# Kernel optimization log

Hardware: AMD Instinct MI355X
Metric: run time of the kernel (lower is better)

Reference implementation:

```python
import jax, jax.numpy as jnp
import numpy as np

# Involution2D config (matches init_kwargs)
F = 256          # filters
K = 3            # kernel_size
G = 16           # groups
RR = 4           # reduce_ratio
BN_EPS = 1e-3    # keras BatchNormalization default epsilon


def setup_inputs() -> dict:
    key = jax.random.key(0)
    ks = jax.random.split(key, 8)
    C = 256
    Cr = F // RR                    # reduce_mapping channels = 64
    KKG = K * K * G                 # span_mapping channels = 144
    s = lambda k, sh, fan: jax.random.normal(k, sh, jnp.float32) * (1.0 / np.sqrt(fan))
    return {
        "x": jax.random.normal(ks[0], (4, 128, 128, C), jnp.float32),
        # reduce_mapping: 1x1 conv + BN(inference) + relu
        "Wr": s(ks[1], (C, Cr), C),
        "br": jnp.zeros((Cr,), jnp.float32),
        "gamma": jnp.ones((Cr,), jnp.float32),
        "beta": jnp.zeros((Cr,), jnp.float32),
        "mean": jax.random.normal(ks[2], (Cr,), jnp.float32) * 0.1,
        "var": jax.random.uniform(ks[3], (Cr,), jnp.float32, 0.5, 1.5),
        # span_mapping: 1x1 conv -> K*K*G dynamic weights
        "Ws": s(ks[4], (Cr, KKG), Cr),
        "bs": jnp.zeros((KKG,), jnp.float32),
        # initial_mapping: 1x1 conv -> F (applied since F != K*K*G)
        "Wi": s(ks[5], (C, F), C),
        "bi": jnp.zeros((F,), jnp.float32),
    }


def reference(x, Wr, br, gamma, beta, mean, var, Ws, bs, Wi, bi):
    B, H, W, _ = x.shape
    KK = K * K
    # reduce_mapping: 1x1 conv + BN(inference) + relu
    r = jnp.einsum('bhwc,cd->bhwd', x, Wr) + br
    r = jax.nn.relu((r - mean) * jax.lax.rsqrt(var + BN_EPS) * gamma + beta)
    # span_mapping: per-pixel dynamic kernel weights [B,H,W,KK*G] -> [B,H,W,G,1,KK]
    w = jnp.einsum('bhwd,dk->bhwk', r, Ws) + bs
    w = w.reshape(B, H, W, G, KK)[:, :, :, :, None, :]
    # initial_mapping: 1x1 conv -> F channels
    xi = jnp.einsum('bhwc,cf->bhwf', x, Wi) + bi
    # tf.image.extract_patches (SAME, stride=1, rate=1): layout is
    # (kernel_pos major, channel minor), i.e. flat index = kpos*F + c
    pad = (K - 1) // 2
    xp = jnp.pad(xi, ((0, 0), (pad, pad), (pad, pad), (0, 0)))
    patches = jnp.stack(
        [xp[:, i:i + H, j:j + W, :] for i in range(K) for j in range(K)],
        axis=3)                                   # [B,H,W,KK,F]
    # faithful to the original K.reshape of the flat [KK*F] axis
    patches = patches.reshape(B, H, W, G, F // G, KK)
    out = jnp.sum(w * patches, axis=-1)           # [B,H,W,G,F//G]
    return out.reshape(B, H, W, F)
```

## Files before the change

### kernel.cpp

```cpp
#include <hip/hip_runtime.h>

#define BN_EPS 1e-3f

typedef __attribute__((ext_vector_type(8))) short bf16x8;
typedef __attribute__((ext_vector_type(4))) float f32x4;

__device__ inline unsigned short f2b(float f) {
    unsigned int u = __float_as_uint(f);
    unsigned int r = (u + 0x7fffu + ((u >> 16) & 1u)) >> 16;
    return (unsigned short)r;
}
__device__ inline float b2f(unsigned short h) {
    return __uint_as_float(((unsigned int)h) << 16);
}
__device__ inline unsigned int pk2(float a, float b) {
    unsigned int r;
    asm("v_cvt_pk_bf16_f32 %0, %1, %2" : "=v"(r) : "v"(a), "v"(b));
    return r;
}
__device__ inline float dot2bf(unsigned int x, unsigned int w, float acc) {
    float r;
    asm("v_dot2_f32_bf16 %0, %1, %2, %3" : "=v"(r) : "v"(x), "v"(w), "v"(acc));
    return r;
}

__global__ void k_prep(const float* __restrict__ Wi, const float* __restrict__ Wr,
                       const float* __restrict__ Ws,
                       unsigned short* __restrict__ Bt, unsigned short* __restrict__ Wst) {
    int t = blockIdx.x * 256 + threadIdx.x;
    if (t < 320 * 256) {
        int n = t >> 8, k = t & 255;
        float v = (n < 256) ? Wi[k * 256 + n] : Wr[k * 64 + (n - 256)];
        Bt[t] = f2b(v);
    } else {
        int t2 = t - 320 * 256;
        if (t2 < 144 * 64) {
            int n = t2 >> 6, k = t2 & 63;
            Wst[t2] = f2b(Ws[k * 144 + n]);
        }
    }
}

__device__ __forceinline__ void gather8(const int* dwp, const unsigned* pkA,
                                        const unsigned* pkB, float w0f, float w8f,
                                        float* res) {
#pragma unroll
    for (int ff = 0; ff < 8; ++ff) {
        const int e0 = ff * 9;
        float a;
        if ((ff & 1) == 0) {
            const int d0 = e0 >> 1;
            a = __uint_as_float(((unsigned)dwp[d0 + 4]) << 16) * w8f;
            a = dot2bf((unsigned)dwp[d0 + 0], pkA[0], a);
            a = dot2bf((unsigned)dwp[d0 + 1], pkA[1], a);
            a = dot2bf((unsigned)dwp[d0 + 2], pkA[2], a);
            a = dot2bf((unsigned)dwp[d0 + 3], pkA[3], a);
        } else {
            const int di = e0 >> 1;
            const int d1 = di + 1;
            a = __uint_as_float(((unsigned)dwp[di]) & 0xffff0000u) * w0f;
            a = dot2bf((unsigned)dwp[d1 + 0], pkB[0], a);
            a = dot2bf((unsigned)dwp[d1 + 1], pkB[1], a);
            a = dot2bf((unsigned)dwp[d1 + 2], pkB[2], a);
            a = dot2bf((unsigned)dwp[d1 + 3], pkB[3], a);
        }
        res[ff] = a;
    }
}

#define XIP 264
#define RS_OFF (180 * XIP)
#define RSP 72
#define WL_OFF (RS_OFF + 180 * RSP)
#define SMN (WL_OFF + 128 * 144)

__global__ __launch_bounds__(512, 2) void k_fused(
    const float* __restrict__ x, const unsigned short* __restrict__ Bt,
    const unsigned short* __restrict__ Wst,
    const float* __restrict__ bi, const float* __restrict__ br,
    const float* __restrict__ gamma, const float* __restrict__ beta,
    const float* __restrict__ mean, const float* __restrict__ var,
    const float* __restrict__ bs, float* __restrict__ out)
{
    __shared__ __attribute__((aligned(16))) unsigned short sm[SMN];
    const int tid = threadIdx.x;
    const int bx = blockIdx.x;
    const int w0 = (bx & 7) * 16;
    const int h0 = ((bx >> 3) & 15) * 8;
    const int bb = bx >> 7;

    const int wv = tid >> 6;
    const int lane = tid & 63;
    const int col = lane & 15;
    const int quad = lane >> 4;

    const float bi_v0 = bi[(2 * wv) * 16 + col];
    const float bi_v1 = bi[(2 * wv + 1) * 16 + col];
    const int dcl = (wv & 3) * 16 + col;
    const float brd = br[dcl];
    const float md  = mean[dcl];
    const float sc  = gamma[dcl] * rsqrtf(var[dcl] + BN_EPS);
    const float btv = beta[dcl];

    bf16x8 bx0[8], bx1[8], brr[8];
    {
        const unsigned short* p0 = &Bt[((2 * wv) * 16 + col) * 256];
        const unsigned short* p1 = &Bt[((2 * wv + 1) * 16 + col) * 256];
#pragma unroll
        for (int kc = 0; kc < 8; ++kc) {
            bx0[kc] = *(const bf16x8*)&p0[kc * 32 + quad * 8];
            bx1[kc] = *(const bf16x8*)&p1[kc * 32 + quad * 8];
        }
        if (wv < 4) {
            const unsigned short* pr = &Bt[((16 + wv) * 16 + col) * 256];
#pragma unroll
            for (int kc = 0; kc < 8; ++kc)
                brr[kc] = *(const bf16x8*)&pr[kc * 32 + quad * 8];
        }
    }

    const int chq = (tid & 15) * 4;

#pragma unroll
    for (int pc = 0; pc < 2; ++pc) {
        float4 vcur[4];
        const int hp = pc * 32 + (tid >> 4);
        int r = hp / 18, cc = hp - r * 18;
        int gh = h0 - 1 + r, gw = w0 - 1 + cc;
        bool ok = ((unsigned)gh < 128u) && ((unsigned)gw < 128u);
        if (ok) {
            const float* src = x + (((long long)(bb * 128 + gh)) * 128 + gw) * 256 + chq;
#pragma unroll
            for (int j = 0; j < 4; ++j) vcur[j] = *(const float4*)&src[j * 64];
        } else {
#pragma unroll
            for (int j = 0; j < 4; ++j) vcur[j] = (float4){0.f, 0.f, 0.f, 0.f};
        }
#pragma unroll
        for (int j = 0; j < 4; ++j) {
            uint2 pk;
            pk.x = pk2(vcur[j].x, vcur[j].y);
            pk.y = pk2(vcur[j].z, vcur[j].w);
            *(uint2*)&sm[hp * XIP + chq + j * 64] = pk;
        }
    }
    __syncthreads();

    for (int c = 0; c < 6; ++c) {
        float4 vn[4];
        int hp_n = 200;
        if (c < 4) {
            hp_n = (c + 2) * 32 + (tid >> 4);
            int r = hp_n / 18, cc = hp_n - r * 18;
            int gh = h0 - 1 + r, gw = w0 - 1 + cc;
            bool ok = (hp_n < 180) && ((unsigned)gh < 128u) && ((unsigned)gw < 128u);
            if (ok) {
                const float* src = x + (((long long)(bb * 128 + gh)) * 128 + gw) * 256 + chq;
#pragma unroll
                for (int j = 0; j < 4; ++j) vn[j] = *(const float4*)&src[j * 64];
            } else {
#pragma unroll
                for (int j = 0; j < 4; ++j) vn[j] = (float4){0.f, 0.f, 0.f, 0.f};
            }
        }

        f32x4 a00 = {0.f,0.f,0.f,0.f}, a01 = a00, a10 = a00, a11 = a00;
        f32x4 ar0 = a00, ar1 = a00;
        {
            const int rowA0 = (c * 32 + col) * XIP;
            const int rowA1 = (c * 32 + 16 + col) * XIP;
#pragma unroll
            for (int kc = 0; kc < 8; ++kc) {
                const int kb = kc * 32 + quad * 8;
                bf16x8 a0 = *(const bf16x8*)&sm[rowA0 + kb];
                bf16x8 a1 = *(const bf16x8*)&sm[rowA1 + kb];
                a00 = __builtin_amdgcn_mfma_f32_16x16x32_bf16(a0, bx0[kc], a00, 0, 0, 0);
                a10 = __builtin_amdgcn_mfma_f32_16x16x32_bf16(a1, bx0[kc], a10, 0, 0, 0);
                a01 = __builtin_amdgcn_mfma_f32_16x16x32_bf16(a0, bx1[kc], a01, 0, 0, 0);
                a11 = __builtin_amdgcn_mfma_f32_16x16x32_bf16(a1, bx1[kc], a11, 0, 0, 0);
                if (wv < 4) {
                    ar0 = __builtin_amdgcn_mfma_f32_16x16x32_bf16(a0, brr[kc], ar0, 0, 0, 0);
                    ar1 = __builtin_amdgcn_mfma_f32_16x16x32_bf16(a1, brr[kc], ar1, 0, 0, 0);
                }
            }
        }
        __syncthreads();

        {
            const int n0 = (2 * wv) * 16 + col;
            const int n1 = (2 * wv + 1) * 16 + col;
            const int rb = c * 32 + quad * 4;
#pragma unroll
            for (int rg = 0; rg < 4; ++rg) {
                const int r0 = rb + rg, r1 = rb + 16 + rg;
                if (r0 < 180) {
                    const unsigned int u0 = pk2(a00[rg] + bi_v0, a01[rg] + bi_v1);
                    sm[r0 * XIP + n0] = (unsigned short)u0;
                    sm[r0 * XIP + n1] = (unsigned short)(u0 >> 16);
                }
                if (r1 < 180) {
                    const unsigned int u1 = pk2(a10[rg] + bi_v0, a11[rg] + bi_v1);
                    sm[r1 * XIP + n0] = (unsigned short)u1;
                    sm[r1 * XIP + n1] = (unsigned short)(u1 >> 16);
                }
            }
            if (wv < 4) {
#pragma unroll
                for (int rg = 0; rg < 4; ++rg) {
                    const int r0 = rb + rg, r1 = rb + 16 + rg;
                    if (r0 < 180) {
                        float v = (ar0[rg] + brd - md) * sc + btv;
                        sm[RS_OFF + r0 * RSP + dcl] = f2b(fmaxf(v, 0.f));
                    }
                    if (r1 < 180) {
                        float v = (ar1[rg] + brd - md) * sc + btv;
                        sm[RS_OFF + r1 * RSP + dcl] = f2b(fmaxf(v, 0.f));
                    }
                }
            }
        }

        if (c < 4 && hp_n < 180) {
#pragma unroll
            for (int j = 0; j < 4; ++j) {
                uint2 pk;
                pk.x = pk2(vn[j].x, vn[j].y);
                pk.y = pk2(vn[j].z, vn[j].w);
                *(uint2*)&sm[hp_n * XIP + chq + j * 64] = pk;
            }
        }
    }
    __syncthreads();

    {
        f32x4 wacc[9];
#pragma unroll
        for (int j = 0; j < 9; ++j) wacc[j] = (f32x4){0.f, 0.f, 0.f, 0.f};
        const int arow = (19 + wv * 18 + col) * RSP;
#pragma unroll
        for (int kc = 0; kc < 2; ++kc) {
            const int kb = kc * 32 + quad * 8;
            bf16x8 ra = *(const bf16x8*)&sm[RS_OFF + arow + kb];
#pragma unroll
            for (int j = 0; j < 9; ++j) {
                bf16x8 wb = *(const bf16x8*)&Wst[(j * 16 + col) * 64 + kb];
                wacc[j] = __builtin_amdgcn_mfma_f32_16x16x32_bf16(ra, wb, wacc[j], 0, 0, 0);
            }
        }
        const int prow = wv * 16 + quad * 4;
#pragma unroll
        for (int j = 0; j < 8; j += 2) {
            const int na = j * 16 + col;
            const int nb = na + 16;
            const float bva = bs[na];
            const float bvb = bs[nb];
#pragma unroll
            for (int rg = 0; rg < 4; ++rg) {
                const unsigned int u = pk2(wacc[j][rg] + bva, wacc[j + 1][rg] + bvb);
                sm[WL_OFF + (prow + rg) * 144 + na] = (unsigned short)u;
                sm[WL_OFF + (prow + rg) * 144 + nb] = (unsigned short)(u >> 16);
            }
        }
        {
            const int n = 8 * 16 + col;
            const float bv = bs[n];
#pragma unroll
            for (int rg = 0; rg < 4; ++rg)
                sm[WL_OFF + (prow + rg) * 144 + n] = f2b(wacc[8][rg] + bv);
        }
    }
    __syncthreads();

    {
        const int g = tid & 15;
        const int pb = tid >> 4;

        const int idx0 = g * 144;
        const int kp0  = idx0 >> 8;
        const int c0   = idx0 & 255;
        int len1 = 256 - c0; if (len1 > 144) len1 = 144;
        const int kp1  = kp0 + 1;
        const int koff0 = (kp0 / 3) * 18 + (kp0 % 3);
        const int koff1 = (kp1 <= 8) ? ((kp1 / 3) * 18 + (kp1 % 3)) : 0;

#pragma unroll
        for (int jj = 0; jj < 4; ++jj) {
            const int p = pb + 32 * jj;
            const int phb = (p >> 4) * 18 + (p & 15);
            const int base0 = (phb + koff0) * XIP + c0;
            const int base1 = (phb + koff1) * XIP;

            unsigned wsv[9];
#pragma unroll
            for (int kk = 0; kk < 9; ++kk)
                wsv[kk] = sm[WL_OFF + p * 144 + g * 9 + kk];
            unsigned pkA[4], pkB[4];
#pragma unroll
            for (int k = 0; k < 4; ++k) {
                pkA[k] = (wsv[2 * k + 1] << 16) | wsv[2 * k];
                pkB[k] = (wsv[2 * k + 2] << 16) | wsv[2 * k + 1];
            }
            const float w0f = __uint_as_float(wsv[0] << 16);
            const float w8f = __uint_as_float(wsv[8] << 16);

            float res[16];
            {
                int4 xv[9];
#pragma unroll
                for (int i = 0; i < 9; ++i) {
                    const int e = i * 8;
                    const int addr = (e < len1) ? (base0 + e) : (base1 + (e - len1));
                    xv[i] = *(const int4*)&sm[addr];
                }
                gather8((const int*)xv, pkA, pkB, w0f, w8f, res);
            }
            {
                int4 xv[9];
#pragma unroll
                for (int i = 9; i < 18; ++i) {
                    const int e = i * 8;
                    const int addr = (e < len1) ? (base0 + e) : (base1 + (e - len1));
                    xv[i - 9] = *(const int4*)&sm[addr];
                }
                gather8((const int*)xv, pkA, pkB, w0f, w8f, res + 8);
            }

            const long long orow =
                (((long long)(bb * 128 + h0 + (p >> 4))) * 128 + (w0 + (p & 15))) * 256 + g * 16;
#pragma unroll
            for (int q = 0; q < 4; ++q) {
                float4 o = {res[q * 4 + 0], res[q * 4 + 1], res[q * 4 + 2], res[q * 4 + 3]};
                *(float4*)&out[orow + q * 4] = o;
            }
        }
    }
}

extern "C" void kernel_launch(void* const* d_in, const int* in_sizes, int n_in,
                              void* d_out, int out_size, void* d_ws, size_t ws_size,
                              hipStream_t stream) {
    const float* x     = (const float*)d_in[0];
    const float* Wr    = (const float*)d_in[1];
    const float* br    = (const float*)d_in[2];
    const float* gamma = (const float*)d_in[3];
    const float* beta  = (const float*)d_in[4];
    const float* mean  = (const float*)d_in[5];
    const float* var   = (const float*)d_in[6];
    const float* Ws    = (const float*)d_in[7];
    const float* bs    = (const float*)d_in[8];
    const float* Wi    = (const float*)d_in[9];
    const float* bi    = (const float*)d_in[10];
    float* out = (float*)d_out;

    unsigned char* ws = (unsigned char*)d_ws;
    unsigned short* Bt  = (unsigned short*)(ws + 0);
    unsigned short* Wst = (unsigned short*)(ws + 163840);

    k_prep<<<dim3(356), dim3(256), 0, stream>>>(Wi, Wr, Ws, Bt, Wst);
    k_fused<<<dim3(512), dim3(512), 0, stream>>>(
        x, Bt, Wst, bi, br, gamma, beta, mean, var, bs, out);
}
```

Measured before the change: 171.8 us.

## Double block size to 1024 threads and split work across twice as many waves

```diff
diff --git a/kernel.cpp b/kernel.cpp
--- a/kernel.cpp
+++ b/kernel.cpp
@@ -74,7 +74,7 @@
 #define WL_OFF (RS_OFF + 180 * RSP)
 #define SMN (WL_OFF + 128 * 144)
 
-__global__ __launch_bounds__(512, 2) void k_fused(
+__global__ __launch_bounds__(1024, 4) void k_fused(
     const float* __restrict__ x, const unsigned short* __restrict__ Bt,
     const unsigned short* __restrict__ Wst,
     const float* __restrict__ bi, const float* __restrict__ br,
@@ -93,10 +93,12 @@
     const int lane = tid & 63;
     const int col = lane & 15;
     const int quad = lane >> 4;
-
-    const float bi_v0 = bi[(2 * wv) * 16 + col];
-    const float bi_v1 = bi[(2 * wv + 1) * 16 + col];
-    const int dcl = (wv & 3) * 16 + col;
+    const int mrow = wv & 1;
+    const int nt = wv >> 1;
+
+    const float bi_v0 = bi[(2 * nt) * 16 + col];
+    const float bi_v1 = bi[(2 * nt + 1) * 16 + col];
+    const int dcl = (nt & 3) * 16 + col;
     const float brd = br[dcl];
     const float md  = mean[dcl];
     const float sc  = gamma[dcl] * rsqrtf(var[dcl] + BN_EPS);
@@ -104,169 +106,162 @@
 
     bf16x8 bx0[8], bx1[8], brr[8];
     {
-        const unsigned short* p0 = &Bt[((2 * wv) * 16 + col) * 256];
-        const unsigned short* p1 = &Bt[((2 * wv + 1) * 16 + col) * 256];
+        const unsigned short* p0 = &Bt[((2 * nt) * 16 + col) * 256];
+        const unsigned short* p1 = &Bt[((2 * nt + 1) * 16 + col) * 256];
 #pragma unroll
         for (int kc = 0; kc < 8; ++kc) {
             bx0[kc] = *(const bf16x8*)&p0[kc * 32 + quad * 8];
             bx1[kc] = *(const bf16x8*)&p1[kc * 32 + quad * 8];
         }
-        if (wv < 4) {
-            const unsigned short* pr = &Bt[((16 + wv) * 16 + col) * 256];
+        if (wv < 8) {
+            const unsigned short* pr = &Bt[((16 + nt) * 16 + col) * 256];
 #pragma unroll
             for (int kc = 0; kc < 8; ++kc)
                 brr[kc] = *(const bf16x8*)&pr[kc * 32 + quad * 8];
         }
     }
 
-    const int chq = (tid & 15) * 4;
+    const int chq = (tid & 31) * 4;
+    const int hpt = tid >> 5;
 
 #pragma unroll
     for (int pc = 0; pc < 2; ++pc) {
-        float4 vcur[4];
-        const int hp = pc * 32 + (tid >> 4);
+        const int hp = pc * 32 + hpt;
         int r = hp / 18, cc = hp - r * 18;
         int gh = h0 - 1 + r, gw = w0 - 1 + cc;
         bool ok = ((unsigned)gh < 128u) && ((unsigned)gw < 128u);
+        float4 v0, v1;
         if (ok) {
             const float* src = x + (((long long)(bb * 128 + gh)) * 128 + gw) * 256 + chq;
-#pragma unroll
-            for (int j = 0; j < 4; ++j) vcur[j] = *(const float4*)&src[j * 64];
+            v0 = *(const float4*)&src[0];
+            v1 = *(const float4*)&src[128];
         } else {
-#pragma unroll
-            for (int j = 0; j < 4; ++j) vcur[j] = (float4){0.f, 0.f, 0.f, 0.f};
-        }
-#pragma unroll
-        for (int j = 0; j < 4; ++j) {
-            uint2 pk;
-            pk.x = pk2(vcur[j].x, vcur[j].y);
-            pk.y = pk2(vcur[j].z, vcur[j].w);
-            *(uint2*)&sm[hp * XIP + chq + j * 64] = pk;
-        }
+            v0 = (float4){0.f, 0.f, 0.f, 0.f};
+            v1 = v0;
+        }
+        uint2 pk;
+        pk.x = pk2(v0.x, v0.y);
+        pk.y = pk2(v0.z, v0.w);
+        *(uint2*)&sm[hp * XIP + chq] = pk;
+        pk.x = pk2(v1.x, v1.y);
+        pk.y = pk2(v1.z, v1.w);
+        *(uint2*)&sm[hp * XIP + chq + 128] = pk;
     }
     __syncthreads();
 
     for (int c = 0; c < 6; ++c) {
-        float4 vn[4];
+        float4 vn0, vn1;
         int hp_n = 200;
         if (c < 4) {
-            hp_n = (c + 2) * 32 + (tid >> 4);
+            hp_n = (c + 2) * 32 + hpt;
             int r = hp_n / 18, cc = hp_n - r * 18;
             int gh = h0 - 1 + r, gw = w0 - 1 + cc;
             bool ok = (hp_n < 180) && ((unsigned)gh < 128u) && ((unsigned)gw < 128u);
             if (ok) {
                 const float* src = x + (((long long)(bb * 128 + gh)) * 128 + gw) * 256 + chq;
-#pragma unroll
-                for (int j = 0; j < 4; ++j) vn[j] = *(const float4*)&src[j * 64];
+                vn0 = *(const float4*)&src[0];
+                vn1 = *(const float4*)&src[128];
             } else {
-#pragma unroll
-                for (int j = 0; j < 4; ++j) vn[j] = (float4){0.f, 0.f, 0.f, 0.f};
-            }
-        }
-
-        f32x4 a00 = {0.f,0.f,0.f,0.f}, a01 = a00, a10 = a00, a11 = a00;
-        f32x4 ar0 = a00, ar1 = a00;
+                vn0 = (float4){0.f, 0.f, 0.f, 0.f};
+                vn1 = vn0;
+            }
+        }
+
+        f32x4 a00 = {0.f,0.f,0.f,0.f}, a01 = a00, ar = a00;
         {
-            const int rowA0 = (c * 32 + col) * XIP;
-            const int rowA1 = (c * 32 + 16 + col) * XIP;
+            const int rowA = (c * 32 + mrow * 16 + col) * XIP;
 #pragma unroll
             for (int kc = 0; kc < 8; ++kc) {
                 const int kb = kc * 32 + quad * 8;
-                bf16x8 a0 = *(const bf16x8*)&sm[rowA0 + kb];
-                bf16x8 a1 = *(const bf16x8*)&sm[rowA1 + kb];
-                a00 = __builtin_amdgcn_mfma_f32_16x16x32_bf16(a0, bx0[kc], a00, 0, 0, 0);
-                a10 = __builtin_amdgcn_mfma_f32_16x16x32_bf16(a1, bx0[kc], a10, 0, 0, 0);
-                a01 = __builtin_amdgcn_mfma_f32_16x16x32_bf16(a0, bx1[kc], a01, 0, 0, 0);
-                a11 = __builtin_amdgcn_mfma_f32_16x16x32_bf16(a1, bx1[kc], a11, 0, 0, 0);
-                if (wv < 4) {
-                    ar0 = __builtin_amdgcn_mfma_f32_16x16x32_bf16(a0, brr[kc], ar0, 0, 0, 0);
-                    ar1 = __builtin_amdgcn_mfma_f32_16x16x32_bf16(a1, brr[kc], ar1, 0, 0, 0);
-                }
+                bf16x8 a = *(const bf16x8*)&sm[rowA + kb];
+                a00 = __builtin_amdgcn_mfma_f32_16x16x32_bf16(a, bx0[kc], a00, 0, 0, 0);
+                a01 = __builtin_amdgcn_mfma_f32_16x16x32_bf16(a, bx1[kc], a01, 0, 0, 0);
+                if (wv < 8)
+                    ar = __builtin_amdgcn_mfma_f32_16x16x32_bf16(a, brr[kc], ar, 0, 0, 0);
             }
         }
         __syncthreads();
 
         {
-            const int n0 = (2 * wv) * 16 + col;
-            const int n1 = (2 * wv + 1) * 16 + col;
-            const int rb = c * 32 + quad * 4;
+            const int n0 = (2 * nt) * 16 + col;
+            const int n1 = n0 + 16;
+            const int rb = c * 32 + mrow * 16 + quad * 4;
 #pragma unroll
             for (int rg = 0; rg < 4; ++rg) {
-                const int r0 = rb + rg, r1 = rb + 16 + rg;
+                const int r0 = rb + rg;
                 if (r0 < 180) {
                     const unsigned int u0 = pk2(a00[rg] + bi_v0, a01[rg] + bi_v1);
                     sm[r0 * XIP + n0] = (unsigned short)u0;
                     sm[r0 * XIP + n1] = (unsigned short)(u0 >> 16);
                 }
-                if (r1 < 180) {
-                    const unsigned int u1 = pk2(a10[rg] + bi_v0, a11[rg] + bi_v1);
-                    sm[r1 * XIP + n0] = (unsigned short)u1;
-                    sm[r1 * XIP + n1] = (unsigned short)(u1 >> 16);
-                }
-            }
-            if (wv < 4) {
+            }
+            if (wv < 8) {
 #pragma unroll
                 for (int rg = 0; rg < 4; ++rg) {
-                    const int r0 = rb + rg, r1 = rb + 16 + rg;
+                    const int r0 = rb + rg;
                     if (r0 < 180) {
-                        float v = (ar0[rg] + brd - md) * sc + btv;
+                        float v = (ar[rg] + brd - md) * sc + btv;
                         sm[RS_OFF + r0 * RSP + dcl] = f2b(fmaxf(v, 0.f));
                     }
-                    if (r1 < 180) {
-                        float v = (ar1[rg] + brd - md) * sc + btv;
-                        sm[RS_OFF + r1 * RSP + dcl] = f2b(fmaxf(v, 0.f));
-                    }
                 }
             }
         }
 
         if (c < 4 && hp_n < 180) {
-#pragma unroll
-            for (int j = 0; j < 4; ++j) {
-                uint2 pk;
-                pk.x = pk2(vn[j].x, vn[j].y);
-                pk.y = pk2(vn[j].z, vn[j].w);
-                *(uint2*)&sm[hp_n * XIP + chq + j * 64] = pk;
-            }
+            uint2 pk;
+            pk.x = pk2(vn0.x, vn0.y);
+            pk.y = pk2(vn0.z, vn0.w);
+            *(uint2*)&sm[hp_n * XIP + chq] = pk;
+            pk.x = pk2(vn1.x, vn1.y);
+            pk.y = pk2(vn1.z, vn1.w);
+            *(uint2*)&sm[hp_n * XIP + chq + 128] = pk;
         }
     }
     __syncthreads();
 
     {
-        f32x4 wacc[9];
-#pragma unroll
-        for (int j = 0; j < 9; ++j) wacc[j] = (f32x4){0.f, 0.f, 0.f, 0.f};
-        const int arow = (19 + wv * 18 + col) * RSP;
+        const int mt = wv >> 1;
+        const int jh = wv & 1;
+        const int jb = jh * 5;
+        const int njt = 5 - jh;
+        f32x4 wacc[5];
+#pragma unroll
+        for (int jj = 0; jj < 5; ++jj) wacc[jj] = (f32x4){0.f, 0.f, 0.f, 0.f};
+        const int arow = (19 + mt * 18 + col) * RSP;
 #pragma unroll
         for (int kc = 0; kc < 2; ++kc) {
             const int kb = kc * 32 + quad * 8;
             bf16x8 ra = *(const bf16x8*)&sm[RS_OFF + arow + kb];
 #pragma unroll
-            for (int j = 0; j < 9; ++j) {
-                bf16x8 wb = *(const bf16x8*)&Wst[(j * 16 + col) * 64 + kb];
-                wacc[j] = __builtin_amdgcn_mfma_f32_16x16x32_bf16(ra, wb, wacc[j], 0, 0, 0);
-            }
-        }
-        const int prow = wv * 16 + quad * 4;
-#pragma unroll
-        for (int j = 0; j < 8; j += 2) {
-            const int na = j * 16 + col;
-            const int nb = na + 16;
-            const float bva = bs[na];
-            const float bvb = bs[nb];
-#pragma unroll
-            for (int rg = 0; rg < 4; ++rg) {
-                const unsigned int u = pk2(wacc[j][rg] + bva, wacc[j + 1][rg] + bvb);
-                sm[WL_OFF + (prow + rg) * 144 + na] = (unsigned short)u;
-                sm[WL_OFF + (prow + rg) * 144 + nb] = (unsigned short)(u >> 16);
-            }
-        }
-        {
-            const int n = 8 * 16 + col;
+            for (int jj = 0; jj < 5; ++jj) {
+                if (jj < njt) {
+                    bf16x8 wb = *(const bf16x8*)&Wst[((jb + jj) * 16 + col) * 64 + kb];
+                    wacc[jj] = __builtin_amdgcn_mfma_f32_16x16x32_bf16(ra, wb, wacc[jj], 0, 0, 0);
+                }
+            }
+        }
+        const int prow = mt * 16 + quad * 4;
+#pragma unroll
+        for (int jj = 0; jj + 1 < 5; jj += 2) {
+            if (jj + 1 < njt) {
+                const int na = (jb + jj) * 16 + col;
+                const int nb = na + 16;
+                const float bva = bs[na];
+                const float bvb = bs[nb];
+#pragma unroll
+                for (int rg = 0; rg < 4; ++rg) {
+                    const unsigned int u = pk2(wacc[jj][rg] + bva, wacc[jj + 1][rg] + bvb);
+                    sm[WL_OFF + (prow + rg) * 144 + na] = (unsigned short)u;
+                    sm[WL_OFF + (prow + rg) * 144 + nb] = (unsigned short)(u >> 16);
+                }
+            }
+        }
+        if (njt & 1) {
+            const int n = (jb + njt - 1) * 16 + col;
             const float bv = bs[n];
 #pragma unroll
             for (int rg = 0; rg < 4; ++rg)
-                sm[WL_OFF + (prow + rg) * 144 + n] = f2b(wacc[8][rg] + bv);
+                sm[WL_OFF + (prow + rg) * 144 + n] = f2b(wacc[njt - 1][rg] + bv);
         }
     }
     __syncthreads();
@@ -284,8 +279,8 @@
         const int koff1 = (kp1 <= 8) ? ((kp1 / 3) * 18 + (kp1 % 3)) : 0;
 
 #pragma unroll
-        for (int jj = 0; jj < 4; ++jj) {
-            const int p = pb + 32 * jj;
+        for (int jj = 0; jj < 2; ++jj) {
+            const int p = pb + 64 * jj;
             const int phb = (p >> 4) * 18 + (p & 15);
             const int base0 = (phb + koff0) * XIP + c0;
             const int base1 = (phb + koff1) * XIP;
@@ -357,6 +352,6 @@
     unsigned short* Wst = (unsigned short*)(ws + 163840);
 
     k_prep<<<dim3(356), dim3(256), 0, stream>>>(Wi, Wr, Ws, Bt, Wst);
-    k_fused<<<dim3(512), dim3(512), 0, stream>>>(
+    k_fused<<<dim3(512), dim3(1024), 0, stream>>>(
         x, Bt, Wst, bi, br, gamma, beta, mean, var, bs, out);
 }
```

Result: slower. 203.2 us (+18.3%).
